# Performance work log

Hardware: AMD Instinct MI355X
Metric: run time of the kernel (lower is better)

## Reference

```python
import jax, jax.numpy as jnp
import numpy as np

B, T, IN, H, L = 128, 2048, 32, 256, 16

def setup_inputs() -> dict:
    key = jax.random.key(0)
    ks = jax.random.split(key, 7)
    s_ih = 1.0 / np.sqrt(IN)
    s_hh = 1.0 / np.sqrt(H)
    return {
        "input_gru": jax.random.normal(ks[0], (B, T, IN), jnp.float32),
        "input_linear": jax.random.normal(ks[1], (B, T, L), jnp.float32),
        "init_hidden": jax.random.normal(ks[2], (B, H), jnp.float32) * 0.1,
        "Wih": jax.random.normal(ks[3], (3 * H, IN), jnp.float32) * s_ih,
        "Whh": jax.random.normal(ks[4], (3 * H, H), jnp.float32) * s_hh,
        "bias": jax.random.normal(ks[5], (3 * H,), jnp.float32) * s_hh,
        "bias_n": jax.random.normal(ks[6], (H,), jnp.float32) * s_hh,
    }

def reference(input_gru, input_linear, init_hidden, Wih, Whh, bias, bias_n):
    # Precompute input-side gate pre-activations for all timesteps: [B,T,3H]
    igates_all = jnp.einsum('bti,gi->btg', input_gru, Wih) + bias
    ig = jnp.moveaxis(igates_all, 1, 0)        # [T,B,3H]
    xl = jnp.moveaxis(input_linear, 1, 0)      # [T,B,L]

    def step(h, inp):
        ig_t, xl_t = inp
        hg = h @ Whh.T                          # [B,3H]
        ir, iz, inew = jnp.split(ig_t, 3, axis=-1)
        hr, hz, hnew = jnp.split(hg, 3, axis=-1)
        r = jax.nn.sigmoid(ir + hr)
        z = jax.nn.sigmoid(iz + hz)             # equinox 'inp' gate
        n = jnp.tanh(inew + r * (hnew + bias_n))
        h_new = n + z * (h - n)                 # equinox GRUCell update
        # dynamic linear readout: params = first L hidden units
        out = jnp.sum(h_new[:, :L] * xl_t, axis=-1, keepdims=True)  # [B,1]
        return h_new, out

    _, outs = jax.lax.scan(step, init_hidden, (ig, xl))  # outs: [T,B,1]
    return jnp.moveaxis(outs, 0, 1)                      # [B,T,1]
```

## Files before the change

kernel.cpp:

```cpp
#include <hip/hip_runtime.h>


typedef _Float16 half8 __attribute__((ext_vector_type(8)));
typedef float float4v __attribute__((ext_vector_type(4)));

#define TT 2048
#define LOG2E 1.44269504088896f

__device__ __forceinline__ float sigm(float x) {
    return __builtin_amdgcn_rcpf(1.f + __builtin_amdgcn_exp2f(-LOG2E * x));
}
__device__ __forceinline__ float tanhf_(float x) {
    float e = __builtin_amdgcn_exp2f(2.f * LOG2E * x);
    return 1.f - 2.f * __builtin_amdgcn_rcpf(e + 1.f);
}

__launch_bounds__(512)
__global__ void gru_kernel(const float* __restrict__ xg,
                           const float* __restrict__ xlin,
                           const float* __restrict__ h0,
                           const float* __restrict__ Wih,
                           const float* __restrict__ Whh,
                           const float* __restrict__ bias,
                           const float* __restrict__ biasn,
                           float* __restrict__ out)
{
    __shared__ _Float16 ldsW[24576];
    __shared__ _Float16 ldsH[2][256];

    const int tid  = threadIdx.x;
    const int b    = blockIdx.x;
    const int lane = tid & 63;
    const int w    = tid >> 6;
    const int l15  = lane & 15;
    const int lhi  = lane >> 4;

    half8 Wh[6][7], Wx[6];
#pragma unroll
    for (int nt = 0; nt < 6; ++nt) {
        const int gtile = 2 * w + (nt >> 1) * 16 + (nt & 1);
        const int row = gtile * 16 + l15;
#pragma unroll
        for (int kt = 0; kt < 7; ++kt) {
            const float4v* pp = (const float4v*)(Whh + row * 256 + kt * 32 + lhi * 8);
            float4v u = pp[0], v2 = pp[1];
            half8 hv;
#pragma unroll
            for (int j = 0; j < 4; ++j) { hv[j] = (_Float16)u[j]; hv[4 + j] = (_Float16)v2[j]; }
            Wh[nt][kt] = hv;
        }
        const float4v* qq = (const float4v*)(Wih + row * 32 + lhi * 8);
        float4v u = qq[0], v2 = qq[1];
        half8 hv;
#pragma unroll
        for (int j = 0; j < 4; ++j) { hv[j] = (_Float16)u[j]; hv[4 + j] = (_Float16)v2[j]; }
        Wx[nt] = hv;
    }

    for (int c = tid; c < 3072; c += 512) {
        int n  = c >> 2;
        int qc = c & 3;
        const float* p = Whh + n * 256 + 224 + qc * 8;
        half8 v;
#pragma unroll
        for (int j = 0; j < 8; ++j) v[j] = (_Float16)p[j];
        *(half8*)((char*)ldsW + qc * 12288 + n * 16) = v;
    }

    float br[2], bz[2], bi[2], bn2[2], hreg[2];
#pragma unroll
    for (int q = 0; q < 2; ++q) {
        const int c = w * 32 + q * 16 + l15;
        br[q]  = bias[c];
        bz[q]  = bias[256 + c];
        bi[q]  = bias[512 + c];
        bn2[q] = biasn[c];
        hreg[q] = h0[b * 256 + c];
    }
    if (tid < 256) ldsH[0][tid] = (_Float16)h0[b * 256 + tid];

    const float* xgb = xg + (size_t)b * TT * 32;
    half8 ax;
    {
        const float4v* px = (const float4v*)(xgb + lhi * 8);
        float4v u = px[0], v2 = px[1];
#pragma unroll
        for (int j = 0; j < 4; ++j) { ax[j] = (_Float16)u[j]; ax[4 + j] = (_Float16)v2[j]; }
    }
    float xlc = 0.f;
    if (w == 0 && lane < 16) xlc = xlin[(size_t)b * TT * 16 + lane];

    __syncthreads();

    const int wb = lhi * 12288 + l15 * 16 + w * 512;
    const float4v zero4 = {0.f, 0.f, 0.f, 0.f};

#pragma clang loop unroll(disable)
    for (int t = 0; t < TT; ++t) {
        const int p  = t & 1;
        const int tn = (t < TT - 1) ? t + 1 : t;

        const float4v* px = (const float4v*)(xgb + (size_t)tn * 32 + lhi * 8);
        float4v xa = px[0], xb2 = px[1];
        float xln = 0.f;
        if (w == 0 && lane < 16) xln = xlin[((size_t)b * TT + tn) * 16 + lane];

        float4v acc[6];
        float xn[2];
#pragma unroll
        for (int nt = 0; nt < 6; ++nt) {
            float4v xq = __builtin_amdgcn_mfma_f32_16x16x32_f16(ax, Wx[nt], zero4, 0, 0, 0);
            if (nt >= 4) { xn[nt - 4] = xq[0]; acc[nt] = zero4; }
            else         { acc[nt] = xq; }
        }
#pragma unroll
        for (int kt = 0; kt < 8; ++kt) {
            half8 a = ((const half8*)ldsH[p])[kt * 4 + lhi];
#pragma unroll
            for (int nt = 0; nt < 6; ++nt) {
                half8 bb;
                if (kt < 7) {
                    bb = Wh[nt][kt];
                } else {
                    const int gtile = 2 * w + (nt >> 1) * 16 + (nt & 1);
                    bb = *(const half8*)((const char*)ldsW + wb + (gtile - 2 * w) * 256);
                    (void)gtile;
                }
                acc[nt] = __builtin_amdgcn_mfma_f32_16x16x32_f16(a, bb, acc[nt], 0, 0, 0);
            }
        }

#pragma unroll
        for (int q = 0; q < 2; ++q) {
            float r = sigm(acc[q][0] + br[q]);
            float z = sigm(acc[2 + q][0] + bz[q]);
            float n = tanhf_(xn[q] + bi[q] + r * (acc[4 + q][0] + bn2[q]));
            float hnew = n + z * (hreg[q] - n);
            hreg[q] = hnew;
            if (lane < 16) ldsH[p ^ 1][w * 32 + q * 16 + l15] = (_Float16)hnew;
        }

        if (w == 0) {
            float v = hreg[0] * xlc;
            v += __shfl_xor(v, 8, 16);
            v += __shfl_xor(v, 4, 16);
            v += __shfl_xor(v, 2, 16);
            v += __shfl_xor(v, 1, 16);
            if (lane == 0) out[(size_t)b * TT + t] = v;
        }

#pragma unroll
        for (int j = 0; j < 4; ++j) { ax[j] = (_Float16)xa[j]; ax[4 + j] = (_Float16)xb2[j]; }
        xlc = xln;
        __syncthreads();
    }
}

extern "C" void kernel_launch(void* const* d_in, const int* in_sizes, int n_in,
                              void* d_out, int out_size, void* d_ws, size_t ws_size,
                              hipStream_t stream) {
    const float* xg    = (const float*)d_in[0];
    const float* xlin  = (const float*)d_in[1];
    const float* h0    = (const float*)d_in[2];
    const float* Wih   = (const float*)d_in[3];
    const float* Whh   = (const float*)d_in[4];
    const float* bias  = (const float*)d_in[5];
    const float* biasn = (const float*)d_in[6];
    float* out = (float*)d_out;

    gru_kernel<<<128, 512, 0, stream>>>(xg, xlin, h0, Wih, Whh, bias, biasn, out);
}
```

Measured before the change: 2.921 ms.

## Halve workgroup to 4 waves holding all Whh in registers, Wih in LDS

Each workgroup drops from 8 to 4 waves, so each wave now covers 64 hidden units (12 gate tiles). The whole Whh slice, all 8 k-tiles, lives in registers (96 half8 values), and the Wih fragments move from registers to LDS. This removes the per-step LDS reads for the last Whh k-tile and makes the per-step barrier cheaper with fewer waves. In exchange each wave issues twice as many MFMAs per step on the serial recurrence critical path and needs very high register use, with a risk of spills.

```diff
diff --git a/kernel.cpp b/kernel.cpp
--- a/kernel.cpp
+++ b/kernel.cpp
@@ -15,7 +15,7 @@
     return 1.f - 2.f * __builtin_amdgcn_rcpf(e + 1.f);
 }
 
-__launch_bounds__(512)
+__attribute__((amdgpu_flat_work_group_size(256, 256), amdgpu_waves_per_eu(1, 1)))
 __global__ void gru_kernel(const float* __restrict__ xg,
                            const float* __restrict__ xlin,
                            const float* __restrict__ h0,
@@ -25,7 +25,7 @@
                            const float* __restrict__ biasn,
                            float* __restrict__ out)
 {
-    __shared__ _Float16 ldsW[24576];
+    __shared__ _Float16 ldsWx[24576];
     __shared__ _Float16 ldsH[2][256];
 
     const int tid  = threadIdx.x;
@@ -35,13 +35,13 @@
     const int l15  = lane & 15;
     const int lhi  = lane >> 4;
 
-    half8 Wh[6][7], Wx[6];
+    half8 Wh[12][8];
 #pragma unroll
-    for (int nt = 0; nt < 6; ++nt) {
-        const int gtile = 2 * w + (nt >> 1) * 16 + (nt & 1);
+    for (int nt = 0; nt < 12; ++nt) {
+        const int gtile = (nt >> 2) * 16 + w * 4 + (nt & 3);
         const int row = gtile * 16 + l15;
 #pragma unroll
-        for (int kt = 0; kt < 7; ++kt) {
+        for (int kt = 0; kt < 8; ++kt) {
             const float4v* pp = (const float4v*)(Whh + row * 256 + kt * 32 + lhi * 8);
             float4v u = pp[0], v2 = pp[1];
             half8 hv;
@@ -49,35 +49,28 @@
             for (int j = 0; j < 4; ++j) { hv[j] = (_Float16)u[j]; hv[4 + j] = (_Float16)v2[j]; }
             Wh[nt][kt] = hv;
         }
-        const float4v* qq = (const float4v*)(Wih + row * 32 + lhi * 8);
-        float4v u = qq[0], v2 = qq[1];
-        half8 hv;
-#pragma unroll
-        for (int j = 0; j < 4; ++j) { hv[j] = (_Float16)u[j]; hv[4 + j] = (_Float16)v2[j]; }
-        Wx[nt] = hv;
     }
 
-    for (int c = tid; c < 3072; c += 512) {
-        int n  = c >> 2;
-        int qc = c & 3;
-        const float* p = Whh + n * 256 + 224 + qc * 8;
+    for (int c = tid; c < 3072; c += 256) {
+        const int row = c >> 2, qc = c & 3;
+        const float* p = Wih + row * 32 + qc * 8;
         half8 v;
 #pragma unroll
         for (int j = 0; j < 8; ++j) v[j] = (_Float16)p[j];
-        *(half8*)((char*)ldsW + qc * 12288 + n * 16) = v;
+        *(half8*)((char*)ldsWx + (((row >> 4) * 64) + qc * 16 + (row & 15)) * 16) = v;
     }
 
-    float br[2], bz[2], bi[2], bn2[2], hreg[2];
+    float br[4], bz[4], bi[4], bn4[4], hreg[4];
 #pragma unroll
-    for (int q = 0; q < 2; ++q) {
-        const int c = w * 32 + q * 16 + l15;
+    for (int q = 0; q < 4; ++q) {
+        const int c = w * 64 + q * 16 + l15;
         br[q]  = bias[c];
         bz[q]  = bias[256 + c];
         bi[q]  = bias[512 + c];
-        bn2[q] = biasn[c];
+        bn4[q] = biasn[c];
         hreg[q] = h0[b * 256 + c];
     }
-    if (tid < 256) ldsH[0][tid] = (_Float16)h0[b * 256 + tid];
+    ldsH[0][tid] = (_Float16)h0[b * 256 + tid];
 
     const float* xgb = xg + (size_t)b * TT * 32;
     half8 ax;
@@ -92,7 +85,6 @@
 
     __syncthreads();
 
-    const int wb = lhi * 12288 + l15 * 16 + w * 512;
     const float4v zero4 = {0.f, 0.f, 0.f, 0.f};
 
 #pragma clang loop unroll(disable)
@@ -105,39 +97,32 @@
         float xln = 0.f;
         if (w == 0 && lane < 16) xln = xlin[((size_t)b * TT + tn) * 16 + lane];
 
-        float4v acc[6];
-        float xn[2];
+        float4v acc[12];
+        float xn4[4];
 #pragma unroll
-        for (int nt = 0; nt < 6; ++nt) {
-            float4v xq = __builtin_amdgcn_mfma_f32_16x16x32_f16(ax, Wx[nt], zero4, 0, 0, 0);
-            if (nt >= 4) { xn[nt - 4] = xq[0]; acc[nt] = zero4; }
+        for (int nt = 0; nt < 12; ++nt) {
+            const int gtile = (nt >> 2) * 16 + w * 4 + (nt & 3);
+            half8 wx = *(const half8*)((const char*)ldsWx + gtile * 1024 + lhi * 256 + l15 * 16);
+            float4v xq = __builtin_amdgcn_mfma_f32_16x16x32_f16(ax, wx, zero4, 0, 0, 0);
+            if (nt >= 8) { xn4[nt - 8] = xq[0]; acc[nt] = zero4; }
             else         { acc[nt] = xq; }
         }
 #pragma unroll
         for (int kt = 0; kt < 8; ++kt) {
             half8 a = ((const half8*)ldsH[p])[kt * 4 + lhi];
 #pragma unroll
-            for (int nt = 0; nt < 6; ++nt) {
-                half8 bb;
-                if (kt < 7) {
-                    bb = Wh[nt][kt];
-                } else {
-                    const int gtile = 2 * w + (nt >> 1) * 16 + (nt & 1);
-                    bb = *(const half8*)((const char*)ldsW + wb + (gtile - 2 * w) * 256);
-                    (void)gtile;
-                }
-                acc[nt] = __builtin_amdgcn_mfma_f32_16x16x32_f16(a, bb, acc[nt], 0, 0, 0);
-            }
+            for (int nt = 0; nt < 12; ++nt)
+                acc[nt] = __builtin_amdgcn_mfma_f32_16x16x32_f16(a, Wh[nt][kt], acc[nt], 0, 0, 0);
         }
 
 #pragma unroll
-        for (int q = 0; q < 2; ++q) {
+        for (int q = 0; q < 4; ++q) {
             float r = sigm(acc[q][0] + br[q]);
-            float z = sigm(acc[2 + q][0] + bz[q]);
-            float n = tanhf_(xn[q] + bi[q] + r * (acc[4 + q][0] + bn2[q]));
+            float z = sigm(acc[4 + q][0] + bz[q]);
+            float n = tanhf_(xn4[q] + bi[q] + r * (acc[8 + q][0] + bn4[q]));
             float hnew = n + z * (hreg[q] - n);
             hreg[q] = hnew;
-            if (lane < 16) ldsH[p ^ 1][w * 32 + q * 16 + l15] = (_Float16)hnew;
+            if (lane < 16) ldsH[p ^ 1][w * 64 + q * 16 + l15] = (_Float16)hnew;
         }
 
         if (w == 0) {
@@ -168,5 +153,5 @@
     const float* biasn = (const float*)d_in[6];
     float* out = (float*)d_out;
 
-    gru_kernel<<<128, 512, 0, stream>>>(xg, xlin, h0, Wih, Whh, bias, biasn, out);
+    gru_kernel<<<128, 256, 0, stream>>>(xg, xlin, h0, Wih, Whh, bias, biasn, out);
 }
```

After: 4.140 ms. 41.7% more time.
